# Kernel optimization log

Hardware: AMD Instinct MI355X
Metric: run time of the kernel (lower is better)

## Reference

```python
import jax, jax.numpy as jnp
import numpy as np

T, B, D, H, O = 1024, 64, 256, 512, 256


def setup_inputs() -> dict:
    key = jax.random.key(0)
    ks = jax.random.split(key, 4)
    s_i = 1.0 / np.sqrt(D)
    s_h = 1.0 / np.sqrt(H)
    return {
        "x": jax.random.normal(ks[0], (T, B, D), jnp.float32),
        "Wi": jax.random.normal(ks[1], (D, 3 * H), jnp.float32) * s_i,
        "bi": jnp.zeros((3 * H,), jnp.float32),
        "Wh": jax.random.normal(ks[2], (H, 3 * H), jnp.float32) * s_h,
        "bhn": jnp.zeros((H,), jnp.float32),
        "Wo": jax.random.normal(ks[3], (H, O), jnp.float32) * s_h,
        "bo": jnp.zeros((O,), jnp.float32),
        "h0": jnp.zeros((B, H), jnp.float32),
    }


def reference(x, Wi, bi, Wh, bhn, Wo, bo, h0):
    # Precompute all input-to-gate projections at once: [T, B, 3H]
    xg = jnp.einsum('tbd,dg->tbg', x, Wi) + bi

    def step(h, xg_t):
        hg = h @ Wh                      # [B, 3H]
        xr, xz, xn = jnp.split(xg_t, 3, axis=-1)
        hr, hz, hn = jnp.split(hg, 3, axis=-1)
        r = jax.nn.sigmoid(xr + hr)
        z = jax.nn.sigmoid(xz + hz)
        n = jnp.tanh(xn + r * (hn + bhn))
        h_new = (1.0 - z) * n + z * h
        return h_new, h_new

    _, hs = jax.lax.scan(step, h0, xg)   # hs: [T, B, H]
    out = jnp.einsum('tbh,ho->tbo', hs, Wo) + bo  # per-step readout
    return out
```

## Files before the change

### kernel.cpp

```cpp
#include <hip/hip_runtime.h>


#define T_ 1024
#define B_ 64
#define D_ 256
#define H_ 512
#define G_ 1536
#define O_ 256

#define SENT 0x7FC0u

typedef __attribute__((ext_vector_type(8))) short short8;
typedef __attribute__((ext_vector_type(4))) short short4v;
typedef __attribute__((ext_vector_type(4))) float float4v;
typedef __attribute__((ext_vector_type(4))) unsigned int uint4v;

static __device__ __forceinline__ unsigned short f2b(float f) {
  unsigned u = __builtin_bit_cast(unsigned, f);
  u += 0x7fffu + ((u >> 16) & 1u);
  return (unsigned short)(u >> 16);
}

__global__ __launch_bounds__(256) void prep_kernel(
    const float* __restrict__ x, const float* __restrict__ Wi,
    const float* __restrict__ Wh, const float* __restrict__ Wo,
    unsigned short* __restrict__ xb, unsigned short* __restrict__ WhT,
    unsigned short* __restrict__ WiT, unsigned short* __restrict__ WoT,
    unsigned short* __restrict__ hs, unsigned* __restrict__ xccbuf)
{
  const size_t NX4 = (size_t)T_ * B_ * D_ / 4;
  const size_t NWH = (size_t)G_ * H_;
  const size_t NWI = (size_t)G_ * D_;
  const size_t NWO = (size_t)O_ * H_;
  const size_t NH8 = (size_t)T_ * B_ * H_ / 8;
  const size_t NXC = 128;
  const size_t NTOT = NX4 + NWH + NWI + NWO + NH8 + NXC;
  size_t i = (size_t)blockIdx.x * blockDim.x + threadIdx.x;
  const size_t stride = (size_t)gridDim.x * blockDim.x;
  for (; i < NTOT; i += stride) {
    if (i < NX4) {
      float4v f = ((const float4v*)x)[i];
      short4v o;
      o[0] = (short)f2b(f[0]); o[1] = (short)f2b(f[1]);
      o[2] = (short)f2b(f[2]); o[3] = (short)f2b(f[3]);
      ((short4v*)xb)[i] = o;
      continue;
    }
    size_t j = i - NX4;
    if (j < NWH) { size_t g = j >> 9, k = j & 511; WhT[j] = f2b(Wh[k * G_ + g]); continue; }
    j -= NWH;
    if (j < NWI) { size_t g = j >> 8, k = j & 255; WiT[j] = f2b(Wi[k * G_ + g]); continue; }
    j -= NWI;
    if (j < NWO) { size_t o = j >> 9, k = j & 511; WoT[j] = f2b(Wo[k * O_ + o]); continue; }
    j -= NWO;
    if (j < NH8) {
      uint4v sv = {0x7FC07FC0u, 0x7FC07FC0u, 0x7FC07FC0u, 0x7FC07FC0u};
      ((uint4v*)hs)[j] = sv;
      continue;
    }
    j -= NH8;
    xccbuf[j] = 0u;
  }
}

__global__ __launch_bounds__(384, 2) void scan_kernel(
    const unsigned short* __restrict__ xb,
    const unsigned short* __restrict__ WhT,
    const unsigned short* __restrict__ WiT,
    unsigned short* __restrict__ hs,
    const float* __restrict__ bi,
    const float* __restrict__ bhn,
    const float* __restrict__ h0,
    unsigned* __restrict__ xccbuf)
{
  const int wg = blockIdx.x;
  const int group = wg & 7;
  if (group >= 4) return;
  const int slice = wg >> 3;
  const int tid = threadIdx.x;
  const int wave = tid >> 6;
  const int lane = tid & 63;
  const int m = lane & 15;
  const int quad = lane >> 4;
  const int gk = wave % 3;
  const int s = wave / 3;
  const int row0 = group * 16;
  const int jbase = slice * 32 + s * 16;
  const int gcol = gk * 512 + jbase + m;

  __shared__ unsigned short hT[16 * 512];
  struct HX { float h, x; };
  __shared__ HX lds_hx[6][256];
  __shared__ unsigned short h_out[16 * 32];
  __shared__ int fast_lds;

  short8 Bh[16], Bx[8];
  {
    const unsigned short* p = WhT + (size_t)gcol * H_ + quad * 8;
#pragma unroll
    for (int k = 0; k < 16; ++k) Bh[k] = *(const short8*)(p + k * 32);
    const unsigned short* q = WiT + (size_t)gcol * D_ + quad * 8;
#pragma unroll
    for (int k = 0; k < 8; ++k) Bx[k] = *(const short8*)(q + k * 32);
  }

  const int jcol = jbase + m;
  const float bi_r = bi[jcol];
  const float bi_z = bi[512 + jcol];
  const float bi_n = bi[1024 + jcol];
  const float bhn_c = bhn[jcol];
  float hold[4];
#pragma unroll
  for (int i = 0; i < 4; ++i)
    hold[i] = h0[(size_t)(row0 + quad * 4 + i) * H_ + jcol];

  for (int i = tid; i < 16 * 512; i += 384) {
    int r = i >> 9, c = i & 511;
    int c2 = (((c >> 3) ^ (r & 7)) << 3) | (c & 7);
    hT[r * 512 + c2] = f2b(h0[(size_t)(row0 + r) * H_ + c]);
  }
  float4v accx = {0.f, 0.f, 0.f, 0.f};
  {
    const unsigned short* xp = xb + ((size_t)0 * B_ + row0 + m) * D_ + quad * 8;
#pragma unroll
    for (int k = 0; k < 8; ++k)
      accx = __builtin_amdgcn_mfma_f32_16x16x32_bf16(*(const short8*)(xp + k * 32), Bx[k], accx, 0, 0, 0);
  }

  {
    unsigned xcc;
    asm("s_getreg_b32 %0, hwreg(HW_REG_XCC_ID)" : "=s"(xcc));
    if (tid == 0) {
      unsigned tok = xcc + 1u;
      unsigned* slot = xccbuf + wg;
      asm volatile("global_store_dword %0, %1, off sc0 sc1"
                   :: "v"(slot), "v"(tok) : "memory");
    }
    if (wave == 0) {
      unsigned v = 0xffffffffu;
      if (lane < 16) {
        const unsigned* p = xccbuf + group + 8 * lane;
        do {
          asm volatile("global_load_dword %0, %1, off sc0 sc1\n\t"
                       "s_waitcnt vmcnt(0)" : "=&v"(v) : "v"(p));
        } while (v == 0u);
      }
      unsigned ref = __shfl(v, 0, 64);
      bool ok = (lane < 16) ? (v == ref) : true;
      if (lane == 0) fast_lds = (__ballot(ok) == ~0ull) ? 1 : 0;
    }
  }
  __syncthreads();
  const bool fast = (fast_lds != 0);

  for (int t = 0; t < T_; ++t) {
    float4v acch0 = {0.f, 0.f, 0.f, 0.f}, acch1 = {0.f, 0.f, 0.f, 0.f};
#pragma unroll
    for (int k = 0; k < 16; k += 2) {
      const int blk0 = (k * 4 + quad) ^ (m & 7);
      short8 a0 = *(const short8*)&hT[m * 512 + blk0 * 8];
      acch0 = __builtin_amdgcn_mfma_f32_16x16x32_bf16(a0, Bh[k], acch0, 0, 0, 0);
      const int blk1 = ((k + 1) * 4 + quad) ^ (m & 7);
      short8 a1 = *(const short8*)&hT[m * 512 + blk1 * 8];
      acch1 = __builtin_amdgcn_mfma_f32_16x16x32_bf16(a1, Bh[k + 1], acch1, 0, 0, 0);
    }
#pragma unroll
    for (int i = 0; i < 4; ++i) {
      const int idx = (quad * 4 + i) * 16 + m;
      HX v; v.h = acch0[i] + acch1[i]; v.x = accx[i];
      lds_hx[wave][idx] = v;
    }
    __syncthreads();
    if (gk == 0) {
      const int wb = s * 3;
#pragma unroll
      for (int i = 0; i < 4; ++i) {
        const int r = quad * 4 + i;
        const int idx = r * 16 + m;
        const HX vr = lds_hx[wb + 0][idx];
        const HX vz = lds_hx[wb + 1][idx];
        const HX vn = lds_hx[wb + 2][idx];
        const float pr = vr.h + vr.x + bi_r;
        const float pz = vz.h + vz.x + bi_z;
        const float rg = 1.f / (1.f + __expf(-pr));
        const float zg = 1.f / (1.f + __expf(-pz));
        const float an = vn.x + bi_n + rg * (vn.h + bhn_c);
        const float e2 = __expf(2.f * an);
        const float ng = 1.f - 2.f / (e2 + 1.f);
        const float hn = (1.f - zg) * ng + zg * hold[i];
        hold[i] = hn;
        h_out[r * 32 + s * 16 + m] = f2b(hn);
      }
    }
    short8 xa[8];
    if (t < T_ - 1) {
      const unsigned short* xp = xb + ((size_t)(t + 1) * B_ + row0 + m) * D_ + quad * 8;
#pragma unroll
      for (int k = 0; k < 8; ++k) xa[k] = *(const short8*)(xp + k * 32);
    }
    __syncthreads();
    if (wave == 1) {
      const int r = lane >> 2, c8 = (lane & 3) * 8;
      short8 hv = *(const short8*)&h_out[r * 32 + c8];
      unsigned short* dst = hs + ((size_t)t * B_ + row0 + r) * H_ + slice * 32 + c8;
      if (fast)
        asm volatile("global_store_dwordx4 %0, %1, off sc0"
                     :: "v"(dst), "v"(hv) : "memory");
      else
        asm volatile("global_store_dwordx4 %0, %1, off sc0 sc1"
                     :: "v"(dst), "v"(hv) : "memory");
    }
    if (t < T_ - 1) {
      const unsigned short* src = hs + ((size_t)t * B_ + row0) * H_;
      const int c0 = tid, c1 = tid + 384;
      const int c2r = tid + 768;
      const int c2 = (c2r < 1024) ? c2r : c0;
      const short8* p0 = (const short8*)(src + (size_t)c0 * 8);
      const short8* p1 = (const short8*)(src + (size_t)c1 * 8);
      const short8* p2 = (const short8*)(src + (size_t)c2 * 8);
      short8 v0, v1, v2;
      bool bad;
      if (fast) {
        do {
          asm volatile(
              "global_load_dwordx4 %0, %3, off sc0\n\t"
              "global_load_dwordx4 %1, %4, off sc0\n\t"
              "global_load_dwordx4 %2, %5, off sc0\n\t"
              "s_waitcnt vmcnt(0)"
              : "=&v"(v0), "=&v"(v1), "=&v"(v2)
              : "v"(p0), "v"(p1), "v"(p2));
          bad = false;
#pragma unroll
          for (int e = 0; e < 8; ++e) {
            bad |= ((unsigned short)v0[e] == (unsigned short)SENT);
            bad |= ((unsigned short)v1[e] == (unsigned short)SENT);
            bad |= ((unsigned short)v2[e] == (unsigned short)SENT);
          }
        } while (bad);
      } else {
        do {
          asm volatile(
              "global_load_dwordx4 %0, %3, off sc0 sc1\n\t"
              "global_load_dwordx4 %1, %4, off sc0 sc1\n\t"
              "global_load_dwordx4 %2, %5, off sc0 sc1\n\t"
              "s_waitcnt vmcnt(0)"
              : "=&v"(v0), "=&v"(v1), "=&v"(v2)
              : "v"(p0), "v"(p1), "v"(p2));
          bad = false;
#pragma unroll
          for (int e = 0; e < 8; ++e) {
            bad |= ((unsigned short)v0[e] == (unsigned short)SENT);
            bad |= ((unsigned short)v1[e] == (unsigned short)SENT);
            bad |= ((unsigned short)v2[e] == (unsigned short)SENT);
          }
        } while (bad);
      }
      { const int r = c0 >> 6, b2 = (c0 & 63) ^ (r & 7); *(short8*)&hT[r * 512 + b2 * 8] = v0; }
      { const int r = c1 >> 6, b2 = (c1 & 63) ^ (r & 7); *(short8*)&hT[r * 512 + b2 * 8] = v1; }
      if (c2r < 1024) { const int r = c2r >> 6, b2 = (c2r & 63) ^ (r & 7); *(short8*)&hT[r * 512 + b2 * 8] = v2; }
      float4v ax0 = {0.f, 0.f, 0.f, 0.f}, ax1 = {0.f, 0.f, 0.f, 0.f};
#pragma unroll
      for (int k = 0; k < 8; k += 2) {
        ax0 = __builtin_amdgcn_mfma_f32_16x16x32_bf16(xa[k], Bx[k], ax0, 0, 0, 0);
        ax1 = __builtin_amdgcn_mfma_f32_16x16x32_bf16(xa[k + 1], Bx[k + 1], ax1, 0, 0, 0);
      }
#pragma unroll
      for (int i = 0; i < 4; ++i) accx[i] = ax0[i] + ax1[i];
      __syncthreads();
    }
  }
}

__global__ __launch_bounds__(256) void ogemm_kernel(
    const unsigned short* __restrict__ hs, const unsigned short* __restrict__ WoT,
    const float* __restrict__ bo, float* __restrict__ out)
{
  const int wv = threadIdx.x >> 6, lane = threadIdx.x & 63;
  const int m = lane & 15, quad = lane >> 4;
  const int rowbase = blockIdx.x * 64 + wv * 16;
  const unsigned short* ap = hs + (size_t)(rowbase + m) * H_ + quad * 8;
  float4v acc[16];
#pragma unroll
  for (int n = 0; n < 16; ++n) { float4v z = {0.f,0.f,0.f,0.f}; acc[n] = z; }
#pragma unroll
  for (int k = 0; k < 16; ++k) {
    short8 a = *(const short8*)(ap + k * 32);
#pragma unroll
    for (int n = 0; n < 16; ++n) {
      short8 b = *(const short8*)(WoT + (size_t)(n * 16 + m) * H_ + k * 32 + quad * 8);
      acc[n] = __builtin_amdgcn_mfma_f32_16x16x32_bf16(a, b, acc[n], 0, 0, 0);
    }
  }
#pragma unroll
  for (int n = 0; n < 16; ++n) {
    const int col = n * 16 + m;
    const float bias = bo[col];
#pragma unroll
    for (int i = 0; i < 4; ++i) {
      const int r = rowbase + quad * 4 + i;
      out[(size_t)r * O_ + col] = acc[n][i] + bias;
    }
  }
}

extern "C" void kernel_launch(void* const* d_in, const int* in_sizes, int n_in,
                              void* d_out, int out_size, void* d_ws, size_t ws_size,
                              hipStream_t stream)
{
  const float* x   = (const float*)d_in[0];
  const float* Wi  = (const float*)d_in[1];
  const float* bi  = (const float*)d_in[2];
  const float* Wh  = (const float*)d_in[3];
  const float* bhn = (const float*)d_in[4];
  const float* Wo  = (const float*)d_in[5];
  const float* bo  = (const float*)d_in[6];
  const float* h0  = (const float*)d_in[7];
  float* out = (float*)d_out;

  char* ws = (char*)d_ws;
  unsigned short* xb  = (unsigned short*)ws;  ws += (size_t)T_ * B_ * D_ * 2;
  unsigned short* WhT = (unsigned short*)ws;  ws += (size_t)G_ * H_ * 2;
  unsigned short* WiT = (unsigned short*)ws;  ws += (size_t)G_ * D_ * 2;
  unsigned short* WoT = (unsigned short*)ws;  ws += (size_t)O_ * H_ * 2;
  unsigned short* hs  = (unsigned short*)ws;  ws += (size_t)T_ * B_ * H_ * 2;
  unsigned* xccbuf    = (unsigned*)ws;

  prep_kernel<<<4096, 256, 0, stream>>>(x, Wi, Wh, Wo, xb, WhT, WiT, WoT, hs, xccbuf);
  scan_kernel<<<128, 384, 0, stream>>>(xb, WhT, WiT, hs, bi, bhn, h0, xccbuf);
  ogemm_kernel<<<1024, 256, 0, stream>>>(hs, WoT, bo, out);
}
```

Before: 3.178 ms.

## Restructure GRU scan to single-wave workgroups computing all three gates per column slice

Each scan workgroup becomes one 64-lane wave covering 16 hidden columns across all three gates, so 128 active workgroups instead of 64. The three gate partial sums stay in registers, which removes the intra-block __syncthreads and the LDS exchange of partials; the input weights move to LDS to make room for the 48 recurrent-weight fragments. The next-step x loads are issued early, the x projection overlaps the spin-wait on h, and the sentinel check compares 32-bit words and retries per lane. In exchange each step has more cross-workgroup polling traffic, and register pressure is much higher.

```diff
diff --git a/kernel.cpp b/kernel.cpp
--- a/kernel.cpp
+++ b/kernel.cpp
@@ -8,7 +8,7 @@
 #define G_ 1536
 #define O_ 256
 
-#define SENT 0x7FC0u
+#define SENT32 0x7FC07FC0u
 
 typedef __attribute__((ext_vector_type(8))) short short8;
 typedef __attribute__((ext_vector_type(4))) short short4v;
@@ -33,7 +33,7 @@
   const size_t NWI = (size_t)G_ * D_;
   const size_t NWO = (size_t)O_ * H_;
   const size_t NH8 = (size_t)T_ * B_ * H_ / 8;
-  const size_t NXC = 128;
+  const size_t NXC = 256;
   const size_t NTOT = NX4 + NWH + NWI + NWO + NH8 + NXC;
   size_t i = (size_t)blockIdx.x * blockDim.x + threadIdx.x;
   const size_t stride = (size_t)gridDim.x * blockDim.x;
@@ -63,7 +63,31 @@
   }
 }
 
-__global__ __launch_bounds__(384, 2) void scan_kernel(
+#define GLOAD16(FLAGS)                                                        \
+  _Pragma("unroll")                                                           \
+  for (int j = 0; j < 16; ++j)                                                \
+    asm volatile("global_load_dwordx4 %0, %1, off " FLAGS                     \
+                 : "=v"(v[j]) : "v"(src8 + j * 64 + lane));
+
+#define FENCE_V16()                                                           \
+  asm volatile("s_waitcnt vmcnt(0)"                                           \
+               : "+v"(v[0]), "+v"(v[1]), "+v"(v[2]), "+v"(v[3]),              \
+                 "+v"(v[4]), "+v"(v[5]), "+v"(v[6]), "+v"(v[7]),              \
+                 "+v"(v[8]), "+v"(v[9]), "+v"(v[10]), "+v"(v[11]),            \
+                 "+v"(v[12]), "+v"(v[13]), "+v"(v[14]), "+v"(v[15])           \
+               :: "memory");                                                  \
+  __builtin_amdgcn_sched_barrier(0);
+
+#define CHECK_V16(BAD)                                                        \
+  BAD = 0u;                                                                   \
+  _Pragma("unroll")                                                           \
+  for (int j = 0; j < 16; ++j) {                                              \
+    uint4v u = __builtin_bit_cast(uint4v, v[j]);                              \
+    BAD |= (unsigned)((u[0] == SENT32) | (u[1] == SENT32) |                   \
+                      (u[2] == SENT32) | (u[3] == SENT32));                   \
+  }
+
+__global__ __launch_bounds__(64, 1) void scan_kernel(
     const unsigned short* __restrict__ xb,
     const unsigned short* __restrict__ WhT,
     const unsigned short* __restrict__ WiT,
@@ -77,34 +101,32 @@
   const int group = wg & 7;
   if (group >= 4) return;
   const int slice = wg >> 3;
-  const int tid = threadIdx.x;
-  const int wave = tid >> 6;
-  const int lane = tid & 63;
+  const int lane = threadIdx.x;
   const int m = lane & 15;
   const int quad = lane >> 4;
-  const int gk = wave % 3;
-  const int s = wave / 3;
   const int row0 = group * 16;
-  const int jbase = slice * 32 + s * 16;
-  const int gcol = gk * 512 + jbase + m;
+  const int jb = slice * 16;
+  const int jcol = jb + m;
 
   __shared__ unsigned short hT[16 * 512];
-  struct HX { float h, x; };
-  __shared__ HX lds_hx[6][256];
-  __shared__ unsigned short h_out[16 * 32];
-  __shared__ int fast_lds;
-
-  short8 Bh[16], Bx[8];
-  {
-    const unsigned short* p = WhT + (size_t)gcol * H_ + quad * 8;
-#pragma unroll
-    for (int k = 0; k < 16; ++k) Bh[k] = *(const short8*)(p + k * 32);
-    const unsigned short* q = WiT + (size_t)gcol * D_ + quad * 8;
-#pragma unroll
-    for (int k = 0; k < 8; ++k) Bx[k] = *(const short8*)(q + k * 32);
-  }
-
-  const int jcol = jbase + m;
+  __shared__ unsigned short BxL[24 * 512];
+  __shared__ unsigned short h_lds[16 * 16];
+
+  short8 Bh[48];
+#pragma unroll
+  for (int g = 0; g < 3; ++g) {
+    const unsigned short* p = WhT + (size_t)(g * 512 + jcol) * H_ + quad * 8;
+#pragma unroll
+    for (int k = 0; k < 16; ++k) Bh[g * 16 + k] = *(const short8*)(p + k * 32);
+  }
+#pragma unroll
+  for (int g = 0; g < 3; ++g) {
+    const unsigned short* q = WiT + (size_t)(g * 512 + jcol) * D_ + quad * 8;
+#pragma unroll
+    for (int k = 0; k < 8; ++k)
+      *(short8*)&BxL[(g * 8 + k) * 512 + lane * 8] = *(const short8*)(q + k * 32);
+  }
+
   const float bi_r = bi[jcol];
   const float bi_z = bi[512 + jcol];
   const float bi_n = bi[1024 + jcol];
@@ -114,95 +136,95 @@
   for (int i = 0; i < 4; ++i)
     hold[i] = h0[(size_t)(row0 + quad * 4 + i) * H_ + jcol];
 
-  for (int i = tid; i < 16 * 512; i += 384) {
-    int r = i >> 9, c = i & 511;
-    int c2 = (((c >> 3) ^ (r & 7)) << 3) | (c & 7);
-    hT[r * 512 + c2] = f2b(h0[(size_t)(row0 + r) * H_ + c]);
-  }
-  float4v accx = {0.f, 0.f, 0.f, 0.f};
-  {
-    const unsigned short* xp = xb + ((size_t)0 * B_ + row0 + m) * D_ + quad * 8;
-#pragma unroll
-    for (int k = 0; k < 8; ++k)
-      accx = __builtin_amdgcn_mfma_f32_16x16x32_bf16(*(const short8*)(xp + k * 32), Bx[k], accx, 0, 0, 0);
-  }
-
+  for (int c = lane; c < 1024; c += 64) {
+    const int r = c >> 6, blk = c & 63;
+    const float* hp = h0 + (size_t)(row0 + r) * H_ + blk * 8;
+    short8 o;
+#pragma unroll
+    for (int j = 0; j < 8; ++j) o[j] = (short)f2b(hp[j]);
+    *(short8*)&hT[r * 512 + ((blk ^ (r & 7))) * 8] = o;
+  }
+
+  bool fast;
   {
     unsigned xcc;
     asm("s_getreg_b32 %0, hwreg(HW_REG_XCC_ID)" : "=s"(xcc));
-    if (tid == 0) {
+    if (lane == 0) {
       unsigned tok = xcc + 1u;
       unsigned* slot = xccbuf + wg;
       asm volatile("global_store_dword %0, %1, off sc0 sc1"
                    :: "v"(slot), "v"(tok) : "memory");
     }
-    if (wave == 0) {
-      unsigned v = 0xffffffffu;
-      if (lane < 16) {
-        const unsigned* p = xccbuf + group + 8 * lane;
-        do {
-          asm volatile("global_load_dword %0, %1, off sc0 sc1\n\t"
-                       "s_waitcnt vmcnt(0)" : "=&v"(v) : "v"(p));
-        } while (v == 0u);
-      }
-      unsigned ref = __shfl(v, 0, 64);
-      bool ok = (lane < 16) ? (v == ref) : true;
-      if (lane == 0) fast_lds = (__ballot(ok) == ~0ull) ? 1 : 0;
-    }
-  }
-  __syncthreads();
-  const bool fast = (fast_lds != 0);
+    unsigned val = 0xffffffffu;
+    if (lane < 32) {
+      const unsigned* p = xccbuf + group + 8 * lane;
+      do {
+        asm volatile("global_load_dword %0, %1, off sc0 sc1\n\t"
+                     "s_waitcnt vmcnt(0)" : "=&v"(val) : "v"(p));
+      } while (val == 0u);
+    }
+    unsigned ref = __shfl(val, 0, 64);
+    bool ok = (lane < 32) ? (val == ref) : true;
+    fast = (__ballot(ok) == ~0ull);
+  }
+
+  asm volatile("s_waitcnt lgkmcnt(0)" ::: "memory");
+  float4v axr = {0.f,0.f,0.f,0.f}, axz = {0.f,0.f,0.f,0.f}, axn = {0.f,0.f,0.f,0.f};
+  {
+    const unsigned short* xp = xb + ((size_t)0 * B_ + row0 + m) * D_ + quad * 8;
+#pragma unroll
+    for (int k = 0; k < 8; ++k) {
+      short8 a = *(const short8*)(xp + k * 32);
+      axr = __builtin_amdgcn_mfma_f32_16x16x32_bf16(a, *(const short8*)&BxL[(0 * 8 + k) * 512 + lane * 8], axr, 0, 0, 0);
+      axz = __builtin_amdgcn_mfma_f32_16x16x32_bf16(a, *(const short8*)&BxL[(1 * 8 + k) * 512 + lane * 8], axz, 0, 0, 0);
+      axn = __builtin_amdgcn_mfma_f32_16x16x32_bf16(a, *(const short8*)&BxL[(2 * 8 + k) * 512 + lane * 8], axn, 0, 0, 0);
+    }
+  }
+  asm volatile("s_waitcnt vmcnt(0) lgkmcnt(0)" ::: "memory");
 
   for (int t = 0; t < T_; ++t) {
-    float4v acch0 = {0.f, 0.f, 0.f, 0.f}, acch1 = {0.f, 0.f, 0.f, 0.f};
+    short8 xa[8];
+    if (t < T_ - 1) {
+      const unsigned short* xp = xb + ((size_t)(t + 1) * B_ + row0 + m) * D_ + quad * 8;
+#pragma unroll
+      for (int k = 0; k < 8; ++k)
+        asm volatile("global_load_dwordx4 %0, %1, off"
+                     : "=v"(xa[k]) : "v"(xp + k * 32));
+    }
+    float4v hr0 = {0.f,0.f,0.f,0.f}, hr1 = {0.f,0.f,0.f,0.f};
+    float4v hz0 = {0.f,0.f,0.f,0.f}, hz1 = {0.f,0.f,0.f,0.f};
+    float4v hn0 = {0.f,0.f,0.f,0.f}, hn1 = {0.f,0.f,0.f,0.f};
 #pragma unroll
     for (int k = 0; k < 16; k += 2) {
       const int blk0 = (k * 4 + quad) ^ (m & 7);
       short8 a0 = *(const short8*)&hT[m * 512 + blk0 * 8];
-      acch0 = __builtin_amdgcn_mfma_f32_16x16x32_bf16(a0, Bh[k], acch0, 0, 0, 0);
+      hr0 = __builtin_amdgcn_mfma_f32_16x16x32_bf16(a0, Bh[k],      hr0, 0, 0, 0);
+      hz0 = __builtin_amdgcn_mfma_f32_16x16x32_bf16(a0, Bh[16 + k], hz0, 0, 0, 0);
+      hn0 = __builtin_amdgcn_mfma_f32_16x16x32_bf16(a0, Bh[32 + k], hn0, 0, 0, 0);
       const int blk1 = ((k + 1) * 4 + quad) ^ (m & 7);
       short8 a1 = *(const short8*)&hT[m * 512 + blk1 * 8];
-      acch1 = __builtin_amdgcn_mfma_f32_16x16x32_bf16(a1, Bh[k + 1], acch1, 0, 0, 0);
+      hr1 = __builtin_amdgcn_mfma_f32_16x16x32_bf16(a1, Bh[k + 1],  hr1, 0, 0, 0);
+      hz1 = __builtin_amdgcn_mfma_f32_16x16x32_bf16(a1, Bh[17 + k], hz1, 0, 0, 0);
+      hn1 = __builtin_amdgcn_mfma_f32_16x16x32_bf16(a1, Bh[33 + k], hn1, 0, 0, 0);
     }
 #pragma unroll
     for (int i = 0; i < 4; ++i) {
-      const int idx = (quad * 4 + i) * 16 + m;
-      HX v; v.h = acch0[i] + acch1[i]; v.x = accx[i];
-      lds_hx[wave][idx] = v;
-    }
-    __syncthreads();
-    if (gk == 0) {
-      const int wb = s * 3;
-#pragma unroll
-      for (int i = 0; i < 4; ++i) {
-        const int r = quad * 4 + i;
-        const int idx = r * 16 + m;
-        const HX vr = lds_hx[wb + 0][idx];
-        const HX vz = lds_hx[wb + 1][idx];
-        const HX vn = lds_hx[wb + 2][idx];
-        const float pr = vr.h + vr.x + bi_r;
-        const float pz = vz.h + vz.x + bi_z;
-        const float rg = 1.f / (1.f + __expf(-pr));
-        const float zg = 1.f / (1.f + __expf(-pz));
-        const float an = vn.x + bi_n + rg * (vn.h + bhn_c);
-        const float e2 = __expf(2.f * an);
-        const float ng = 1.f - 2.f / (e2 + 1.f);
-        const float hn = (1.f - zg) * ng + zg * hold[i];
-        hold[i] = hn;
-        h_out[r * 32 + s * 16 + m] = f2b(hn);
-      }
-    }
-    short8 xa[8];
-    if (t < T_ - 1) {
-      const unsigned short* xp = xb + ((size_t)(t + 1) * B_ + row0 + m) * D_ + quad * 8;
-#pragma unroll
-      for (int k = 0; k < 8; ++k) xa[k] = *(const short8*)(xp + k * 32);
-    }
-    __syncthreads();
-    if (wave == 1) {
-      const int r = lane >> 2, c8 = (lane & 3) * 8;
-      short8 hv = *(const short8*)&h_out[r * 32 + c8];
-      unsigned short* dst = hs + ((size_t)t * B_ + row0 + r) * H_ + slice * 32 + c8;
+      const float pr = hr0[i] + hr1[i] + axr[i] + bi_r;
+      const float pz = hz0[i] + hz1[i] + axz[i] + bi_z;
+      const float rg = 1.f / (1.f + __expf(-pr));
+      const float zg = 1.f / (1.f + __expf(-pz));
+      const float an = axn[i] + bi_n + rg * (hn0[i] + hn1[i] + bhn_c);
+      const float e2 = __expf(2.f * an);
+      const float ng = 1.f - 2.f / (e2 + 1.f);
+      const float hn = (1.f - zg) * ng + zg * hold[i];
+      hold[i] = hn;
+      h_lds[(quad * 4 + i) * 16 + m] = f2b(hn);
+    }
+    asm volatile("s_waitcnt lgkmcnt(0)" ::: "memory");
+    if (lane < 32) {
+      const int r = lane >> 1, half = lane & 1;
+      short8 hv = *(const short8*)&h_lds[r * 16 + half * 8];
+      unsigned short* dst = hs + ((size_t)t * B_ + row0 + r) * H_ + jb + half * 8;
       if (fast)
         asm volatile("global_store_dwordx4 %0, %1, off sc0"
                      :: "v"(dst), "v"(hv) : "memory");
@@ -210,64 +232,41 @@
         asm volatile("global_store_dwordx4 %0, %1, off sc0 sc1"
                      :: "v"(dst), "v"(hv) : "memory");
     }
-    if (t < T_ - 1) {
-      const unsigned short* src = hs + ((size_t)t * B_ + row0) * H_;
-      const int c0 = tid, c1 = tid + 384;
-      const int c2r = tid + 768;
-      const int c2 = (c2r < 1024) ? c2r : c0;
-      const short8* p0 = (const short8*)(src + (size_t)c0 * 8);
-      const short8* p1 = (const short8*)(src + (size_t)c1 * 8);
-      const short8* p2 = (const short8*)(src + (size_t)c2 * 8);
-      short8 v0, v1, v2;
-      bool bad;
-      if (fast) {
-        do {
-          asm volatile(
-              "global_load_dwordx4 %0, %3, off sc0\n\t"
-              "global_load_dwordx4 %1, %4, off sc0\n\t"
-              "global_load_dwordx4 %2, %5, off sc0\n\t"
-              "s_waitcnt vmcnt(0)"
-              : "=&v"(v0), "=&v"(v1), "=&v"(v2)
-              : "v"(p0), "v"(p1), "v"(p2));
-          bad = false;
-#pragma unroll
-          for (int e = 0; e < 8; ++e) {
-            bad |= ((unsigned short)v0[e] == (unsigned short)SENT);
-            bad |= ((unsigned short)v1[e] == (unsigned short)SENT);
-            bad |= ((unsigned short)v2[e] == (unsigned short)SENT);
-          }
-        } while (bad);
-      } else {
-        do {
-          asm volatile(
-              "global_load_dwordx4 %0, %3, off sc0 sc1\n\t"
-              "global_load_dwordx4 %1, %4, off sc0 sc1\n\t"
-              "global_load_dwordx4 %2, %5, off sc0 sc1\n\t"
-              "s_waitcnt vmcnt(0)"
-              : "=&v"(v0), "=&v"(v1), "=&v"(v2)
-              : "v"(p0), "v"(p1), "v"(p2));
-          bad = false;
-#pragma unroll
-          for (int e = 0; e < 8; ++e) {
-            bad |= ((unsigned short)v0[e] == (unsigned short)SENT);
-            bad |= ((unsigned short)v1[e] == (unsigned short)SENT);
-            bad |= ((unsigned short)v2[e] == (unsigned short)SENT);
-          }
-        } while (bad);
+    if (t == T_ - 1) break;
+
+    const short8* src8 = (const short8*)(hs + ((size_t)t * B_ + row0) * H_);
+    short8 v[16];
+    if (fast) { GLOAD16("sc0") } else { GLOAD16("sc0 sc1") }
+
+    asm volatile("s_waitcnt vmcnt(17)"
+                 : "+v"(xa[0]), "+v"(xa[1]), "+v"(xa[2]), "+v"(xa[3]),
+                   "+v"(xa[4]), "+v"(xa[5]), "+v"(xa[6]), "+v"(xa[7])
+                 :: "memory");
+    __builtin_amdgcn_sched_barrier(0);
+    {
+      float4v nr = {0.f,0.f,0.f,0.f}, nz = {0.f,0.f,0.f,0.f}, nn = {0.f,0.f,0.f,0.f};
+#pragma unroll
+      for (int k = 0; k < 8; ++k) {
+        nr = __builtin_amdgcn_mfma_f32_16x16x32_bf16(xa[k], *(const short8*)&BxL[(0 * 8 + k) * 512 + lane * 8], nr, 0, 0, 0);
+        nz = __builtin_amdgcn_mfma_f32_16x16x32_bf16(xa[k], *(const short8*)&BxL[(1 * 8 + k) * 512 + lane * 8], nz, 0, 0, 0);
+        nn = __builtin_amdgcn_mfma_f32_16x16x32_bf16(xa[k], *(const short8*)&BxL[(2 * 8 + k) * 512 + lane * 8], nn, 0, 0, 0);
       }
-      { const int r = c0 >> 6, b2 = (c0 & 63) ^ (r & 7); *(short8*)&hT[r * 512 + b2 * 8] = v0; }
-      { const int r = c1 >> 6, b2 = (c1 & 63) ^ (r & 7); *(short8*)&hT[r * 512 + b2 * 8] = v1; }
-      if (c2r < 1024) { const int r = c2r >> 6, b2 = (c2r & 63) ^ (r & 7); *(short8*)&hT[r * 512 + b2 * 8] = v2; }
-      float4v ax0 = {0.f, 0.f, 0.f, 0.f}, ax1 = {0.f, 0.f, 0.f, 0.f};
-#pragma unroll
-      for (int k = 0; k < 8; k += 2) {
-        ax0 = __builtin_amdgcn_mfma_f32_16x16x32_bf16(xa[k], Bx[k], ax0, 0, 0, 0);
-        ax1 = __builtin_amdgcn_mfma_f32_16x16x32_bf16(xa[k + 1], Bx[k + 1], ax1, 0, 0, 0);
+      axr = nr; axz = nz; axn = nn;
+    }
+    unsigned bad;
+    FENCE_V16();
+    CHECK_V16(bad);
+    while (__any((int)bad)) {
+      if (bad) {
+        if (fast) { GLOAD16("sc0") } else { GLOAD16("sc0 sc1") }
       }
-#pragma unroll
-      for (int i = 0; i < 4; ++i) accx[i] = ax0[i] + ax1[i];
-      __syncthreads();
-    }
+      FENCE_V16();
+      CHECK_V16(bad);
+    }
+#pragma unroll
+    for (int j = 0; j < 16; ++j)
+      *(short8*)&hT[j * 512 + ((lane ^ (j & 7))) * 8] = v[j];
+    asm volatile("s_waitcnt lgkmcnt(0)" ::: "memory");
   }
 }
 
@@ -326,6 +325,6 @@
   unsigned* xccbuf    = (unsigned*)ws;
 
   prep_kernel<<<4096, 256, 0, stream>>>(x, Wi, Wh, Wo, xb, WhT, WiT, WoT, hs, xccbuf);
-  scan_kernel<<<128, 384, 0, stream>>>(xb, WhT, WiT, hs, bi, bhn, h0, xccbuf);
+  scan_kernel<<<256, 64, 0, stream>>>(xb, WhT, WiT, hs, bi, bhn, h0, xccbuf);
   ogemm_kernel<<<1024, 256, 0, stream>>>(hs, WoT, bo, out);
 }
```

After: 3.688 ms. 1.16x slower.

## Spread gate math across all waves and remove the per-step LDS staging barrier

Applied to the files above, without the earlier changes.

Gate computation now runs on all six waves instead of only the gk==0 waves. Each thread writes its bf16 h value straight to global memory with a short store, which removes the h_out LDS staging and one __syncthreads per step. The x-tile prefetch for the next step is issued at the start of the step and waited on with partial vmcnt so it overlaps the recurrent MFMAs. Polling now uses a SWAR sentinel check and reloads only the vectors that are still stale. In exchange it issues many small scattered global stores instead of one vector store per wave, and it relies on hand-counted vmcnt values.

```diff
diff --git a/kernel.cpp b/kernel.cpp
--- a/kernel.cpp
+++ b/kernel.cpp
@@ -8,7 +8,7 @@
 #define G_ 1536
 #define O_ 256
 
-#define SENT 0x7FC0u
+#define SENT32 0x7FC07FC0u
 
 typedef __attribute__((ext_vector_type(8))) short short8;
 typedef __attribute__((ext_vector_type(4))) short short4v;
@@ -33,7 +33,7 @@
   const size_t NWI = (size_t)G_ * D_;
   const size_t NWO = (size_t)O_ * H_;
   const size_t NH8 = (size_t)T_ * B_ * H_ / 8;
-  const size_t NXC = 128;
+  const size_t NXC = 256;
   const size_t NTOT = NX4 + NWH + NWI + NWO + NH8 + NXC;
   size_t i = (size_t)blockIdx.x * blockDim.x + threadIdx.x;
   const size_t stride = (size_t)gridDim.x * blockDim.x;
@@ -62,6 +62,46 @@
     xccbuf[j] = 0u;
   }
 }
+
+
+#define CHKB(V, BAD) do {                                                     \
+    uint4v u_ = __builtin_bit_cast(uint4v, V);                                \
+    unsigned b_ = 0u;                                                         \
+    _Pragma("unroll")                                                         \
+    for (int q_ = 0; q_ < 4; ++q_) {                                          \
+      unsigned x_ = u_[q_] ^ SENT32;                                          \
+      b_ |= (x_ - 0x00010001u) & ~x_ & 0x80008000u;                           \
+    }                                                                         \
+    BAD = b_;                                                                 \
+  } while (0)
+
+#define FENCE3()                                                              \
+  asm volatile("s_waitcnt vmcnt(0)"                                           \
+               : "+v"(v0), "+v"(v1), "+v"(v2) :: "memory");                   \
+  __builtin_amdgcn_sched_barrier(0);
+
+#define POLL(FLAGS)                                                           \
+  asm volatile("global_load_dwordx4 %0, %2, off " FLAGS "\n\t"                \
+               "global_load_dwordx4 %1, %3, off " FLAGS                       \
+               : "=v"(v0), "=v"(v1) : "v"(p0), "v"(p1));                      \
+  if (wave < 4)                                                               \
+    asm volatile("global_load_dwordx4 %0, %1, off " FLAGS                     \
+                 : "=v"(v2) : "v"(p2));                                       \
+  FENCE3();                                                                   \
+  CHKB(v0, bad0); CHKB(v1, bad1);                                             \
+  if (wave < 4) { CHKB(v2, bad2); } else bad2 = 0u;                           \
+  while (__any((int)(bad0 | bad1 | bad2) != 0)) {                             \
+    if (bad0) asm volatile("global_load_dwordx4 %0, %1, off " FLAGS           \
+                           : "=v"(v0) : "v"(p0));                             \
+    if (bad1) asm volatile("global_load_dwordx4 %0, %1, off " FLAGS           \
+                           : "=v"(v1) : "v"(p1));                             \
+    if (bad2) asm volatile("global_load_dwordx4 %0, %1, off " FLAGS           \
+                           : "=v"(v2) : "v"(p2));                             \
+    FENCE3();                                                                 \
+    if (bad0) CHKB(v0, bad0);                                                 \
+    if (bad1) CHKB(v1, bad1);                                                 \
+    if (bad2) CHKB(v2, bad2);                                                 \
+  }
 
 __global__ __launch_bounds__(384, 2) void scan_kernel(
     const unsigned short* __restrict__ xb,
@@ -91,7 +131,6 @@
   __shared__ unsigned short hT[16 * 512];
   struct HX { float h, x; };
   __shared__ HX lds_hx[6][256];
-  __shared__ unsigned short h_out[16 * 32];
   __shared__ int fast_lds;
 
   short8 Bh[16], Bx[8];
@@ -109,10 +148,9 @@
   const float bi_z = bi[512 + jcol];
   const float bi_n = bi[1024 + jcol];
   const float bhn_c = bhn[jcol];
-  float hold[4];
-#pragma unroll
-  for (int i = 0; i < 4; ++i)
-    hold[i] = h0[(size_t)(row0 + quad * 4 + i) * H_ + jcol];
+  const int iA = (gk == 0) ? 0 : gk;
+  float holdA = h0[(size_t)(row0 + quad * 4 + iA) * H_ + jcol];
+  float holdB = (gk == 0) ? h0[(size_t)(row0 + quad * 4 + 3) * H_ + jcol] : 0.f;
 
   for (int i = tid; i < 16 * 512; i += 384) {
     int r = i >> 9, c = i & 511;
@@ -137,23 +175,32 @@
                    :: "v"(slot), "v"(tok) : "memory");
     }
     if (wave == 0) {
-      unsigned v = 0xffffffffu;
+      unsigned val = 0xffffffffu;
       if (lane < 16) {
         const unsigned* p = xccbuf + group + 8 * lane;
         do {
           asm volatile("global_load_dword %0, %1, off sc0 sc1\n\t"
-                       "s_waitcnt vmcnt(0)" : "=&v"(v) : "v"(p));
-        } while (v == 0u);
+                       "s_waitcnt vmcnt(0)" : "=&v"(val) : "v"(p));
+        } while (val == 0u);
       }
-      unsigned ref = __shfl(v, 0, 64);
-      bool ok = (lane < 16) ? (v == ref) : true;
+      unsigned ref = __shfl(val, 0, 64);
+      bool ok = (lane < 16) ? (val == ref) : true;
       if (lane == 0) fast_lds = (__ballot(ok) == ~0ull) ? 1 : 0;
     }
   }
+  asm volatile("s_waitcnt vmcnt(0) lgkmcnt(0)" ::: "memory");
   __syncthreads();
   const bool fast = (fast_lds != 0);
 
   for (int t = 0; t < T_; ++t) {
+    short8 xa[8];
+    if (t < T_ - 1) {
+      const unsigned short* xp = xb + ((size_t)(t + 1) * B_ + row0 + m) * D_ + quad * 8;
+#pragma unroll
+      for (int k = 0; k < 8; ++k)
+        asm volatile("global_load_dwordx4 %0, %1, off"
+                     : "=v"(xa[k]) : "v"(xp + k * 32));
+    }
     float4v acch0 = {0.f, 0.f, 0.f, 0.f}, acch1 = {0.f, 0.f, 0.f, 0.f};
 #pragma unroll
     for (int k = 0; k < 16; k += 2) {
@@ -171,12 +218,10 @@
       lds_hx[wave][idx] = v;
     }
     __syncthreads();
-    if (gk == 0) {
+    {
       const int wb = s * 3;
-#pragma unroll
-      for (int i = 0; i < 4; ++i) {
-        const int r = quad * 4 + i;
-        const int idx = r * 16 + m;
+      auto do_gate = [&](int i, float& hold_ref) {
+        const int idx = (quad * 4 + i) * 16 + m;
         const HX vr = lds_hx[wb + 0][idx];
         const HX vz = lds_hx[wb + 1][idx];
         const HX vn = lds_hx[wb + 2][idx];
@@ -187,77 +232,34 @@
         const float an = vn.x + bi_n + rg * (vn.h + bhn_c);
         const float e2 = __expf(2.f * an);
         const float ng = 1.f - 2.f / (e2 + 1.f);
-        const float hn = (1.f - zg) * ng + zg * hold[i];
-        hold[i] = hn;
-        h_out[r * 32 + s * 16 + m] = f2b(hn);
-      }
-    }
-    short8 xa[8];
-    if (t < T_ - 1) {
-      const unsigned short* xp = xb + ((size_t)(t + 1) * B_ + row0 + m) * D_ + quad * 8;
-#pragma unroll
-      for (int k = 0; k < 8; ++k) xa[k] = *(const short8*)(xp + k * 32);
-    }
-    __syncthreads();
-    if (wave == 1) {
-      const int r = lane >> 2, c8 = (lane & 3) * 8;
-      short8 hv = *(const short8*)&h_out[r * 32 + c8];
-      unsigned short* dst = hs + ((size_t)t * B_ + row0 + r) * H_ + slice * 32 + c8;
-      if (fast)
-        asm volatile("global_store_dwordx4 %0, %1, off sc0"
-                     :: "v"(dst), "v"(hv) : "memory");
-      else
-        asm volatile("global_store_dwordx4 %0, %1, off sc0 sc1"
-                     :: "v"(dst), "v"(hv) : "memory");
-    }
-    if (t < T_ - 1) {
-      const unsigned short* src = hs + ((size_t)t * B_ + row0) * H_;
-      const int c0 = tid, c1 = tid + 384;
-      const int c2r = tid + 768;
-      const int c2 = (c2r < 1024) ? c2r : c0;
-      const short8* p0 = (const short8*)(src + (size_t)c0 * 8);
-      const short8* p1 = (const short8*)(src + (size_t)c1 * 8);
-      const short8* p2 = (const short8*)(src + (size_t)c2 * 8);
-      short8 v0, v1, v2;
-      bool bad;
-      if (fast) {
-        do {
-          asm volatile(
-              "global_load_dwordx4 %0, %3, off sc0\n\t"
-              "global_load_dwordx4 %1, %4, off sc0\n\t"
-              "global_load_dwordx4 %2, %5, off sc0\n\t"
-              "s_waitcnt vmcnt(0)"
-              : "=&v"(v0), "=&v"(v1), "=&v"(v2)
-              : "v"(p0), "v"(p1), "v"(p2));
-          bad = false;
-#pragma unroll
-          for (int e = 0; e < 8; ++e) {
-            bad |= ((unsigned short)v0[e] == (unsigned short)SENT);
-            bad |= ((unsigned short)v1[e] == (unsigned short)SENT);
-            bad |= ((unsigned short)v2[e] == (unsigned short)SENT);
-          }
-        } while (bad);
-      } else {
-        do {
-          asm volatile(
-              "global_load_dwordx4 %0, %3, off sc0 sc1\n\t"
-              "global_load_dwordx4 %1, %4, off sc0 sc1\n\t"
-              "global_load_dwordx4 %2, %5, off sc0 sc1\n\t"
-              "s_waitcnt vmcnt(0)"
-              : "=&v"(v0), "=&v"(v1), "=&v"(v2)
-              : "v"(p0), "v"(p1), "v"(p2));
-          bad = false;
-#pragma unroll
-          for (int e = 0; e < 8; ++e) {
-            bad |= ((unsigned short)v0[e] == (unsigned short)SENT);
-            bad |= ((unsigned short)v1[e] == (unsigned short)SENT);
-            bad |= ((unsigned short)v2[e] == (unsigned short)SENT);
-          }
-        } while (bad);
-      }
-      { const int r = c0 >> 6, b2 = (c0 & 63) ^ (r & 7); *(short8*)&hT[r * 512 + b2 * 8] = v0; }
-      { const int r = c1 >> 6, b2 = (c1 & 63) ^ (r & 7); *(short8*)&hT[r * 512 + b2 * 8] = v1; }
-      if (c2r < 1024) { const int r = c2r >> 6, b2 = (c2r & 63) ^ (r & 7); *(short8*)&hT[r * 512 + b2 * 8] = v2; }
+        const float hn = (1.f - zg) * ng + zg * hold_ref;
+        hold_ref = hn;
+        const unsigned hb = (unsigned)f2b(hn);
+        unsigned short* dst = hs + ((size_t)t * B_ + row0 + quad * 4 + i) * H_ + jcol;
+        if (fast)
+          asm volatile("global_store_short %0, %1, off sc0"
+                       :: "v"(dst), "v"(hb) : "memory");
+        else
+          asm volatile("global_store_short %0, %1, off sc0 sc1"
+                       :: "v"(dst), "v"(hb) : "memory");
+      };
+      do_gate(iA, holdA);
+      if (gk == 0) do_gate(3, holdB);
+    }
+    if (t == T_ - 1) break;
+
+    if (gk == 0)
+      asm volatile("s_waitcnt vmcnt(2)"
+                   : "+v"(xa[0]), "+v"(xa[1]), "+v"(xa[2]), "+v"(xa[3]),
+                     "+v"(xa[4]), "+v"(xa[5]), "+v"(xa[6]), "+v"(xa[7])
+                   :: "memory");
+    else
+      asm volatile("s_waitcnt vmcnt(1)"
+                   : "+v"(xa[0]), "+v"(xa[1]), "+v"(xa[2]), "+v"(xa[3]),
+                     "+v"(xa[4]), "+v"(xa[5]), "+v"(xa[6]), "+v"(xa[7])
+                   :: "memory");
+    __builtin_amdgcn_sched_barrier(0);
+    {
       float4v ax0 = {0.f, 0.f, 0.f, 0.f}, ax1 = {0.f, 0.f, 0.f, 0.f};
 #pragma unroll
       for (int k = 0; k < 8; k += 2) {
@@ -266,8 +268,21 @@
       }
 #pragma unroll
       for (int i = 0; i < 4; ++i) accx[i] = ax0[i] + ax1[i];
-      __syncthreads();
-    }
+    }
+    {
+      const unsigned short* src = hs + ((size_t)t * B_ + row0) * H_;
+      const int c0 = tid, c1 = tid + 384, c2r = tid + 768;
+      const short8* p0 = (const short8*)(src + (size_t)c0 * 8);
+      const short8* p1 = (const short8*)(src + (size_t)c1 * 8);
+      const short8* p2 = (const short8*)(src + (size_t)c2r * 8);
+      short8 v0 = {}, v1 = {}, v2 = {};
+      unsigned bad0, bad1, bad2;
+      if (fast) { POLL("sc0") } else { POLL("sc0 sc1") }
+      { const int r = c0 >> 6, b2 = (c0 & 63) ^ (r & 7); *(short8*)&hT[r * 512 + b2 * 8] = v0; }
+      { const int r = c1 >> 6, b2 = (c1 & 63) ^ (r & 7); *(short8*)&hT[r * 512 + b2 * 8] = v1; }
+      if (wave < 4) { const int r = c2r >> 6, b2 = (c2r & 63) ^ (r & 7); *(short8*)&hT[r * 512 + b2 * 8] = v2; }
+    }
+    __syncthreads();
   }
 }
 
```

New measurement: 3.813 ms. 20.0% more time.
